# Kernel optimization log

Hardware: AMD Instinct MI355X
Metric: run time of the kernel (lower is better)

The kernel has to match this reference:

```python
import jax, jax.numpy as jnp
import numpy as np

NUM_NODES = 10000
NUM_EDGES = 640000
D_FEAT = 128

def setup_inputs() -> dict:
    key = jax.random.key(0)
    k1, k2 = jax.random.split(key)
    x = jax.random.normal(k1, (NUM_NODES, D_FEAT), dtype=jnp.float32)
    edge_index = jax.random.randint(k2, (2, NUM_EDGES), 0, NUM_NODES, dtype=jnp.int64)
    return {"x": x, "edge_index": edge_index}

def reference(x, edge_index):
    # MessagePassing(aggr='add') with default message/update:
    # msg = x[src]; out[n] = sum of msg over edges with dst == n
    src, dst = edge_index[0], edge_index[1]
    msg = x[src]                                   # [num_edges, d]
    out = jax.ops.segment_sum(msg, dst, num_segments=NUM_NODES)  # [num_nodes, d]
    return out
```

## Files before the change

### kernel.cpp

```cpp
#include <hip/hip_runtime.h>

#define NUM_NODES 10000
#define NUM_EDGES 640000
#define D_FEAT 128

#define NPB 20
#define NB 500
#define K1_BLOCKS 256
#define EPB (NUM_EDGES / K1_BLOCKS)
#define CELL_CAP 16
#define MAXB 1792
#define INV 0xFFFFFFFFu
#define ZROW 10000u

#define XB_U4 (NUM_NODES * 16 + 16)
#define CVT_PER_BLOCK (NUM_NODES * 16 / K1_BLOCKS)


__device__ __forceinline__ unsigned bf16_rne(float f) {
    unsigned u = __float_as_uint(f);
    return (u + 0x7FFFu + ((u >> 16) & 1u)) >> 16;
}

__device__ __forceinline__ int div20(int d) {
    return (int)(((unsigned)d * 104858u) >> 21);
}

__global__ __launch_bounds__(1024) void scatter_cvt_kernel(
    const int* __restrict__ ei, const float4* __restrict__ x4,
    uint4* __restrict__ xb, unsigned* __restrict__ ovfcell,
    uint4* __restrict__ slots4)
{
    __shared__ int cur[NB];
    __shared__ uint4 cellsv[NB * (CELL_CAP / 4)];
    __shared__ unsigned s_ovf[15];
    __shared__ int ovfcur;

    int t = threadIdx.x, b = blockIdx.x;
    if (t < NB) cur[t] = 0;
    if (t < 15) s_ovf[t] = 0;
    if (t == 0) ovfcur = 0;
    uint4 iv = make_uint4(INV, INV, INV, INV);
    if (t < 1000) { cellsv[t] = iv; cellsv[t + 1000] = iv; }

    int base = b * EPB;
    int s0 = ei[base + t];
    int d0 = ei[NUM_EDGES + base + t];
    int s1 = ei[base + t + 1024];
    int d1 = ei[NUM_EDGES + base + t + 1024];
    int s2 = 0, d2 = 0;
    bool has2 = (t + 2048) < EPB;
    if (has2) {
        s2 = ei[base + t + 2048];
        d2 = ei[NUM_EDGES + base + t + 2048];
    }

    if (t < CVT_PER_BLOCK) {
        int o = b * CVT_PER_BLOCK + t;
        float4 a = x4[2 * o];
        float4 c = x4[2 * o + 1];
        uint4 w;
        w.x = bf16_rne(a.x) | (bf16_rne(a.y) << 16);
        w.y = bf16_rne(a.z) | (bf16_rne(a.w) << 16);
        w.z = bf16_rne(c.x) | (bf16_rne(c.y) << 16);
        w.w = bf16_rne(c.z) | (bf16_rne(c.w) << 16);
        xb[o] = w;
    }
    if (b == 0 && t < 16)
        xb[NUM_NODES * 16 + t] = make_uint4(0u, 0u, 0u, 0u);
    __syncthreads();

    unsigned* cells = (unsigned*)cellsv;
    {
        int k = div20(d0), m = d0 - k * NPB;
        int pos = atomicAdd(&cur[k], 1);
        if (pos < CELL_CAP)
            cells[k * CELL_CAP + pos] = ((unsigned)m << 16) | (unsigned)s0;
        else {
            int o = atomicAdd(&ovfcur, 1);
            if (o < 15) s_ovf[o] = ((unsigned)k << 19) |
                                   ((unsigned)m << 14) | (unsigned)s0;
        }
    }
    {
        int k = div20(d1), m = d1 - k * NPB;
        int pos = atomicAdd(&cur[k], 1);
        if (pos < CELL_CAP)
            cells[k * CELL_CAP + pos] = ((unsigned)m << 16) | (unsigned)s1;
        else {
            int o = atomicAdd(&ovfcur, 1);
            if (o < 15) s_ovf[o] = ((unsigned)k << 19) |
                                   ((unsigned)m << 14) | (unsigned)s1;
        }
    }
    if (has2) {
        int k = div20(d2), m = d2 - k * NPB;
        int pos = atomicAdd(&cur[k], 1);
        if (pos < CELL_CAP)
            cells[k * CELL_CAP + pos] = ((unsigned)m << 16) | (unsigned)s2;
        else {
            int o = atomicAdd(&ovfcur, 1);
            if (o < 15) s_ovf[o] = ((unsigned)k << 19) |
                                   ((unsigned)m << 14) | (unsigned)s2;
        }
    }
    __syncthreads();

    for (int idx = t; idx < NB * (CELL_CAP / 4); idx += 1024)
        slots4[((unsigned)(idx >> 2) * K1_BLOCKS + (unsigned)b) *
               (CELL_CAP / 4) + (unsigned)(idx & 3)] = cellsv[idx];
    if (t < 15) ovfcell[b * 16 + t] = s_ovf[t];
    if (t == 15) ovfcell[b * 16 + 15] = (unsigned)min(ovfcur, 15);
}

__device__ __forceinline__ void acc8(float* a, uint4 w) {
    a[0] += __uint_as_float(w.x << 16);
    a[1] += __uint_as_float(w.x & 0xFFFF0000u);
    a[2] += __uint_as_float(w.y << 16);
    a[3] += __uint_as_float(w.y & 0xFFFF0000u);
    a[4] += __uint_as_float(w.z << 16);
    a[5] += __uint_as_float(w.z & 0xFFFF0000u);
    a[6] += __uint_as_float(w.w << 16);
    a[7] += __uint_as_float(w.w & 0xFFFF0000u);
}

__device__ __forceinline__ void reduce_write(float* a, int node, int q, int sub,
                                             float4* __restrict__ out4) {
    #pragma unroll
    for (int r = 0; r < 8; ++r) {
        a[r] += __shfl_down(a[r], 32);
        a[r] += __shfl_down(a[r], 16);
    }
    if (q == 0) {
        unsigned o = (unsigned)node * 32u + (unsigned)sub * 2u;
        out4[o]     = make_float4(a[0], a[1], a[2], a[3]);
        out4[o + 1] = make_float4(a[4], a[5], a[6], a[7]);
    }
}

__global__ __launch_bounds__(640, 5) void sort_gather_kernel(
    const uint4* __restrict__ xb,
    const uint4* __restrict__ slots4,
    const unsigned* __restrict__ ovfcell,
    float4* __restrict__ out4)
{
    __shared__ unsigned s_src[MAXB];
    __shared__ int h[NPB];
    __shared__ int off20[NPB];
    __shared__ int cur20[NPB];
    __shared__ int s_ovfany;

    int k = blockIdx.x;
    int t = threadIdx.x;

    if (t < NPB) h[t] = 0;
    if (t == 0) s_ovfany = 0;
    for (int i = t; i < MAXB; i += 640) s_src[i] = ZROW;

    if (t < K1_BLOCKS) {
        unsigned oc = ovfcell[t * 16 + 15];
        if (oc) atomicOr(&s_ovfany, 1);
    }

    const uint4* sb = slots4 + (unsigned)k * 1024u;
    uint4 w40 = sb[t];
    uint4 w41 = (t < 384) ? sb[t + 640] : make_uint4(INV, INV, INV, INV);
    __syncthreads();

    {
        unsigned m;
        m = w40.x >> 16; if (m < NPB) atomicAdd(&h[m], 1);
        m = w40.y >> 16; if (m < NPB) atomicAdd(&h[m], 1);
        m = w40.z >> 16; if (m < NPB) atomicAdd(&h[m], 1);
        m = w40.w >> 16; if (m < NPB) atomicAdd(&h[m], 1);
        m = w41.x >> 16; if (m < NPB) atomicAdd(&h[m], 1);
        m = w41.y >> 16; if (m < NPB) atomicAdd(&h[m], 1);
        m = w41.z >> 16; if (m < NPB) atomicAdd(&h[m], 1);
        m = w41.w >> 16; if (m < NPB) atomicAdd(&h[m], 1);
    }
    if (s_ovfany && t < K1_BLOCKS) {
        int oc = (int)min(ovfcell[t * 16 + 15], 15u);
        for (int i = 0; i < oc; ++i) {
            unsigned e = ovfcell[t * 16 + i];
            if ((int)(e >> 19) == k) atomicAdd(&h[(e >> 14) & 31u], 1);
        }
    }
    __syncthreads();

    if (t < 32) {
        int val = (t < NPB) ? (((h[t] + 3) & ~3) + 4) : 0;
        int s = val;
        #pragma unroll
        for (int d = 1; d < 32; d <<= 1) {
            int u = __shfl_up(s, d, 32);
            if (t >= d) s += u;
        }
        if (t < NPB) { off20[t] = s - val; cur20[t] = s - val; }
    }
    __syncthreads();

    {
        unsigned m;
        m = w40.x >> 16; if (m < NPB) { int p = atomicAdd(&cur20[m], 1); if (p < MAXB) s_src[p] = w40.x & 0xFFFFu; }
        m = w40.y >> 16; if (m < NPB) { int p = atomicAdd(&cur20[m], 1); if (p < MAXB) s_src[p] = w40.y & 0xFFFFu; }
        m = w40.z >> 16; if (m < NPB) { int p = atomicAdd(&cur20[m], 1); if (p < MAXB) s_src[p] = w40.z & 0xFFFFu; }
        m = w40.w >> 16; if (m < NPB) { int p = atomicAdd(&cur20[m], 1); if (p < MAXB) s_src[p] = w40.w & 0xFFFFu; }
        m = w41.x >> 16; if (m < NPB) { int p = atomicAdd(&cur20[m], 1); if (p < MAXB) s_src[p] = w41.x & 0xFFFFu; }
        m = w41.y >> 16; if (m < NPB) { int p = atomicAdd(&cur20[m], 1); if (p < MAXB) s_src[p] = w41.y & 0xFFFFu; }
        m = w41.z >> 16; if (m < NPB) { int p = atomicAdd(&cur20[m], 1); if (p < MAXB) s_src[p] = w41.z & 0xFFFFu; }
        m = w41.w >> 16; if (m < NPB) { int p = atomicAdd(&cur20[m], 1); if (p < MAXB) s_src[p] = w41.w & 0xFFFFu; }
    }
    if (s_ovfany && t < K1_BLOCKS) {
        int oc = (int)min(ovfcell[t * 16 + 15], 15u);
        for (int i = 0; i < oc; ++i) {
            unsigned e = ovfcell[t * 16 + i];
            if ((int)(e >> 19) == k) {
                int p = atomicAdd(&cur20[(e >> 14) & 31u], 1);
                if (p < MAXB) s_src[p] = e & 0x3FFFu;
            }
        }
    }
    __syncthreads();

    int wave = t >> 6;
    int lane = t & 63;
    int q    = lane >> 4;
    int sub  = lane & 15;

    {
        int m = wave;
        int bA = off20[m];
        int eA = (h[m] + 3) & ~3;
        float a[8] = {0.f, 0.f, 0.f, 0.f, 0.f, 0.f, 0.f, 0.f};
        unsigned s = s_src[bA + q];
        uint4 r = xb[s * 16u + (unsigned)sub];
        for (int j = 0; j < eA; j += 4) {
            unsigned s2 = s_src[bA + j + 4 + q];
            uint4 r2 = xb[s2 * 16u + (unsigned)sub];
            acc8(a, r);
            r = r2;
        }
        reduce_write(a, k * NPB + m, q, sub, out4);
    }
    {
        int m = wave + 10;
        int bB = off20[m];
        int eB = (h[m] + 3) & ~3;
        float a[8] = {0.f, 0.f, 0.f, 0.f, 0.f, 0.f, 0.f, 0.f};
        unsigned s = s_src[bB + q];
        uint4 r = xb[s * 16u + (unsigned)sub];
        for (int j = 0; j < eB; j += 4) {
            unsigned s2 = s_src[bB + j + 4 + q];
            uint4 r2 = xb[s2 * 16u + (unsigned)sub];
            acc8(a, r);
            r = r2;
        }
        reduce_write(a, k * NPB + m, q, sub, out4);
    }
}

extern "C" void kernel_launch(void* const* d_in, const int* in_sizes, int n_in,
                              void* d_out, int out_size, void* d_ws, size_t ws_size,
                              hipStream_t stream) {
    const float* x   = (const float*)d_in[0];
    const int*   ei  = (const int*)d_in[1];
    float*       out = (float*)d_out;

    uint4*    xb      = (uint4*)d_ws;
    unsigned* ovfcell = (unsigned*)(xb + XB_U4);
    uint4*    slots4  = (uint4*)(ovfcell + K1_BLOCKS * 16);

    scatter_cvt_kernel<<<K1_BLOCKS, 1024, 0, stream>>>(
        ei, (const float4*)x, xb, ovfcell, slots4);

    sort_gather_kernel<<<NB, 640, 0, stream>>>(
        xb, (const uint4*)slots4, ovfcell, (float4*)out);
}
```

Before: 81.59 us.

## Replace histogram+scan bucketing with fixed per-node stripes and slow-path fallback

Measured after the change: 80.96 us, median of 2. About the same (-0.8%).

```diff
diff --git a/kernel.cpp b/kernel.cpp
--- a/kernel.cpp
+++ b/kernel.cpp
@@ -9,12 +9,16 @@
 #define K1_BLOCKS 256
 #define EPB (NUM_EDGES / K1_BLOCKS)
 #define CELL_CAP 16
-#define MAXB 1792
 #define INV 0xFFFFFFFFu
 #define ZROW 10000u
+#define STRIPE 112
+#define SCAP 108
+#define MAXB (NPB * STRIPE)
 
 #define XB_U4 (NUM_NODES * 16 + 16)
 #define CVT_PER_BLOCK (NUM_NODES * 16 / K1_BLOCKS)
+
+typedef __attribute__((ext_vector_type(2))) float f32x2;
 
 
 __device__ __forceinline__ unsigned bf16_rne(float f) {
@@ -113,29 +117,20 @@
     if (t == 15) ovfcell[b * 16 + 15] = (unsigned)min(ovfcur, 15);
 }
 
-__device__ __forceinline__ void acc8(float* a, uint4 w) {
-    a[0] += __uint_as_float(w.x << 16);
-    a[1] += __uint_as_float(w.x & 0xFFFF0000u);
-    a[2] += __uint_as_float(w.y << 16);
-    a[3] += __uint_as_float(w.y & 0xFFFF0000u);
-    a[4] += __uint_as_float(w.z << 16);
-    a[5] += __uint_as_float(w.z & 0xFFFF0000u);
-    a[6] += __uint_as_float(w.w << 16);
-    a[7] += __uint_as_float(w.w & 0xFFFF0000u);
-}
-
-__device__ __forceinline__ void reduce_write(float* a, int node, int q, int sub,
-                                             float4* __restrict__ out4) {
-    #pragma unroll
-    for (int r = 0; r < 8; ++r) {
-        a[r] += __shfl_down(a[r], 32);
-        a[r] += __shfl_down(a[r], 16);
-    }
-    if (q == 0) {
-        unsigned o = (unsigned)node * 32u + (unsigned)sub * 2u;
-        out4[o]     = make_float4(a[0], a[1], a[2], a[3]);
-        out4[o + 1] = make_float4(a[4], a[5], a[6], a[7]);
-    }
+__device__ __forceinline__ void acc8p(f32x2* a, uint4 w) {
+    f32x2 v;
+    v.x = __uint_as_float(w.x << 16);
+    v.y = __uint_as_float(w.x & 0xFFFF0000u);
+    a[0] += v;
+    v.x = __uint_as_float(w.y << 16);
+    v.y = __uint_as_float(w.y & 0xFFFF0000u);
+    a[1] += v;
+    v.x = __uint_as_float(w.z << 16);
+    v.y = __uint_as_float(w.z & 0xFFFF0000u);
+    a[2] += v;
+    v.x = __uint_as_float(w.w << 16);
+    v.y = __uint_as_float(w.w & 0xFFFF0000u);
+    a[3] += v;
 }
 
 __global__ __launch_bounds__(640, 5) void sort_gather_kernel(
@@ -145,15 +140,13 @@
     float4* __restrict__ out4)
 {
     __shared__ unsigned s_src[MAXB];
-    __shared__ int h[NPB];
-    __shared__ int off20[NPB];
     __shared__ int cur20[NPB];
     __shared__ int s_ovfany;
 
     int k = blockIdx.x;
     int t = threadIdx.x;
 
-    if (t < NPB) h[t] = 0;
+    if (t < NPB) cur20[t] = t * STRIPE;
     if (t == 0) s_ovfany = 0;
     for (int i = t; i < MAXB; i += 640) s_src[i] = ZROW;
 
@@ -169,54 +162,23 @@
 
     {
         unsigned m;
-        m = w40.x >> 16; if (m < NPB) atomicAdd(&h[m], 1);
-        m = w40.y >> 16; if (m < NPB) atomicAdd(&h[m], 1);
-        m = w40.z >> 16; if (m < NPB) atomicAdd(&h[m], 1);
-        m = w40.w >> 16; if (m < NPB) atomicAdd(&h[m], 1);
-        m = w41.x >> 16; if (m < NPB) atomicAdd(&h[m], 1);
-        m = w41.y >> 16; if (m < NPB) atomicAdd(&h[m], 1);
-        m = w41.z >> 16; if (m < NPB) atomicAdd(&h[m], 1);
-        m = w41.w >> 16; if (m < NPB) atomicAdd(&h[m], 1);
-    }
-    if (s_ovfany && t < K1_BLOCKS) {
-        int oc = (int)min(ovfcell[t * 16 + 15], 15u);
-        for (int i = 0; i < oc; ++i) {
-            unsigned e = ovfcell[t * 16 + i];
-            if ((int)(e >> 19) == k) atomicAdd(&h[(e >> 14) & 31u], 1);
-        }
-    }
-    __syncthreads();
-
-    if (t < 32) {
-        int val = (t < NPB) ? (((h[t] + 3) & ~3) + 4) : 0;
-        int s = val;
-        #pragma unroll
-        for (int d = 1; d < 32; d <<= 1) {
-            int u = __shfl_up(s, d, 32);
-            if (t >= d) s += u;
-        }
-        if (t < NPB) { off20[t] = s - val; cur20[t] = s - val; }
-    }
-    __syncthreads();
-
-    {
-        unsigned m;
-        m = w40.x >> 16; if (m < NPB) { int p = atomicAdd(&cur20[m], 1); if (p < MAXB) s_src[p] = w40.x & 0xFFFFu; }
-        m = w40.y >> 16; if (m < NPB) { int p = atomicAdd(&cur20[m], 1); if (p < MAXB) s_src[p] = w40.y & 0xFFFFu; }
-        m = w40.z >> 16; if (m < NPB) { int p = atomicAdd(&cur20[m], 1); if (p < MAXB) s_src[p] = w40.z & 0xFFFFu; }
-        m = w40.w >> 16; if (m < NPB) { int p = atomicAdd(&cur20[m], 1); if (p < MAXB) s_src[p] = w40.w & 0xFFFFu; }
-        m = w41.x >> 16; if (m < NPB) { int p = atomicAdd(&cur20[m], 1); if (p < MAXB) s_src[p] = w41.x & 0xFFFFu; }
-        m = w41.y >> 16; if (m < NPB) { int p = atomicAdd(&cur20[m], 1); if (p < MAXB) s_src[p] = w41.y & 0xFFFFu; }
-        m = w41.z >> 16; if (m < NPB) { int p = atomicAdd(&cur20[m], 1); if (p < MAXB) s_src[p] = w41.z & 0xFFFFu; }
-        m = w41.w >> 16; if (m < NPB) { int p = atomicAdd(&cur20[m], 1); if (p < MAXB) s_src[p] = w41.w & 0xFFFFu; }
+        m = w40.x >> 16; if (m < NPB) { int p = atomicAdd(&cur20[m], 1); if (p < (int)(m * STRIPE + SCAP)) s_src[p] = w40.x & 0xFFFFu; }
+        m = w40.y >> 16; if (m < NPB) { int p = atomicAdd(&cur20[m], 1); if (p < (int)(m * STRIPE + SCAP)) s_src[p] = w40.y & 0xFFFFu; }
+        m = w40.z >> 16; if (m < NPB) { int p = atomicAdd(&cur20[m], 1); if (p < (int)(m * STRIPE + SCAP)) s_src[p] = w40.z & 0xFFFFu; }
+        m = w40.w >> 16; if (m < NPB) { int p = atomicAdd(&cur20[m], 1); if (p < (int)(m * STRIPE + SCAP)) s_src[p] = w40.w & 0xFFFFu; }
+        m = w41.x >> 16; if (m < NPB) { int p = atomicAdd(&cur20[m], 1); if (p < (int)(m * STRIPE + SCAP)) s_src[p] = w41.x & 0xFFFFu; }
+        m = w41.y >> 16; if (m < NPB) { int p = atomicAdd(&cur20[m], 1); if (p < (int)(m * STRIPE + SCAP)) s_src[p] = w41.y & 0xFFFFu; }
+        m = w41.z >> 16; if (m < NPB) { int p = atomicAdd(&cur20[m], 1); if (p < (int)(m * STRIPE + SCAP)) s_src[p] = w41.z & 0xFFFFu; }
+        m = w41.w >> 16; if (m < NPB) { int p = atomicAdd(&cur20[m], 1); if (p < (int)(m * STRIPE + SCAP)) s_src[p] = w41.w & 0xFFFFu; }
     }
     if (s_ovfany && t < K1_BLOCKS) {
         int oc = (int)min(ovfcell[t * 16 + 15], 15u);
         for (int i = 0; i < oc; ++i) {
             unsigned e = ovfcell[t * 16 + i];
             if ((int)(e >> 19) == k) {
-                int p = atomicAdd(&cur20[(e >> 14) & 31u], 1);
-                if (p < MAXB) s_src[p] = e & 0x3FFFu;
+                unsigned m = (e >> 14) & 31u;
+                int p = atomicAdd(&cur20[m], 1);
+                if (p < (int)(m * STRIPE + SCAP)) s_src[p] = e & 0x3FFFu;
             }
         }
     }
@@ -227,35 +189,60 @@
     int q    = lane >> 4;
     int sub  = lane & 15;
 
-    {
-        int m = wave;
-        int bA = off20[m];
-        int eA = (h[m] + 3) & ~3;
-        float a[8] = {0.f, 0.f, 0.f, 0.f, 0.f, 0.f, 0.f, 0.f};
-        unsigned s = s_src[bA + q];
-        uint4 r = xb[s * 16u + (unsigned)sub];
-        for (int j = 0; j < eA; j += 4) {
-            unsigned s2 = s_src[bA + j + 4 + q];
-            uint4 r2 = xb[s2 * 16u + (unsigned)sub];
-            acc8(a, r);
-            r = r2;
-        }
-        reduce_write(a, k * NPB + m, q, sub, out4);
-    }
-    {
-        int m = wave + 10;
-        int bB = off20[m];
-        int eB = (h[m] + 3) & ~3;
-        float a[8] = {0.f, 0.f, 0.f, 0.f, 0.f, 0.f, 0.f, 0.f};
-        unsigned s = s_src[bB + q];
-        uint4 r = xb[s * 16u + (unsigned)sub];
-        for (int j = 0; j < eB; j += 4) {
-            unsigned s2 = s_src[bB + j + 4 + q];
-            uint4 r2 = xb[s2 * 16u + (unsigned)sub];
-            acc8(a, r);
-            r = r2;
-        }
-        reduce_write(a, k * NPB + m, q, sub, out4);
+    #pragma unroll
+    for (int half = 0; half < 2; ++half) {
+        int m = wave + half * 10;
+        int ecRaw = cur20[m] - m * STRIPE;
+        f32x2 a[4];
+        a[0] = 0.f; a[1] = 0.f; a[2] = 0.f; a[3] = 0.f;
+
+        if (ecRaw <= SCAP) {
+            int bA = m * STRIPE;
+            int eA = (ecRaw + 3) & ~3;
+            unsigned s = s_src[bA + q];
+            uint4 r = xb[s * 16u + (unsigned)sub];
+            for (int j = 0; j < eA; j += 4) {
+                unsigned s2 = s_src[bA + j + 4 + q];
+                uint4 r2 = xb[s2 * 16u + (unsigned)sub];
+                acc8p(a, r);
+                r = r2;
+            }
+        } else {
+            const unsigned* sw = (const unsigned*)sb;
+            for (int idx = q; idx < K1_BLOCKS * CELL_CAP; idx += 4) {
+                unsigned w = sw[idx];
+                if ((w >> 16) == (unsigned)m) {
+                    uint4 r = xb[(w & 0xFFFFu) * 16u + (unsigned)sub];
+                    acc8p(a, r);
+                }
+            }
+            if (s_ovfany && q == 0) {
+                for (int bb = 0; bb < K1_BLOCKS; ++bb) {
+                    int oc = (int)min(ovfcell[bb * 16 + 15], 15u);
+                    for (int i = 0; i < oc; ++i) {
+                        unsigned e = ovfcell[bb * 16 + i];
+                        if ((int)(e >> 19) == k &&
+                            (int)((e >> 14) & 31u) == m) {
+                            uint4 r = xb[(e & 0x3FFFu) * 16u + (unsigned)sub];
+                            acc8p(a, r);
+                        }
+                    }
+                }
+            }
+        }
+
+        #pragma unroll
+        for (int r = 0; r < 4; ++r) {
+            a[r].x += __shfl_down(a[r].x, 32);
+            a[r].y += __shfl_down(a[r].y, 32);
+            a[r].x += __shfl_down(a[r].x, 16);
+            a[r].y += __shfl_down(a[r].y, 16);
+        }
+        if (q == 0) {
+            unsigned o = (unsigned)(k * NPB + m) * 32u + (unsigned)sub * 2u;
+            out4[o]     = make_float4(a[0].x, a[0].y, a[1].x, a[1].y);
+            out4[o + 1] = make_float4(a[2].x, a[2].y, a[3].x, a[3].y);
+        }
     }
 }
 
```
